# Optimization experiments

Hardware: AMD Instinct MI355X
Metric: run time of the kernel (lower is better)

The kernel has to match this reference:

```python
import jax, jax.numpy as jnp
import numpy as np

GAMMA = 1.0

def _rbf_mean(X, Y, gamma):
    x2 = jnp.sum(X * X, axis=1)  # [n]
    y2 = jnp.sum(Y * Y, axis=1)  # [m]
    d2 = x2[:, None] + y2[None, :] - 2.0 * (X @ Y.T)
    d2 = jnp.maximum(d2, 0.0)
    return jnp.mean(jnp.exp(-gamma * d2))

def setup_inputs() -> dict:
    key = jax.random.key(0)
    k1, k2 = jax.random.split(key)
    N = jax.random.normal(k1, (8192, 256), dtype=jnp.float32)
    R = jax.random.normal(k2, (8192, 256), dtype=jnp.float32)
    return {"N": N, "R": R}

def reference(N, R):
    xx = _rbf_mean(N, N, GAMMA)
    yy = _rbf_mean(R, R, GAMMA)
    xy = _rbf_mean(N, R, GAMMA)
    mmd = xx + yy - 2.0 * xy
    return jnp.sqrt(mmd)
```

## Files before the change

### kernel.cpp

```cpp
#include <hip/hip_runtime.h>
#include <math.h>

typedef float f32x4 __attribute__((ext_vector_type(4)));
typedef int   i32x4 __attribute__((ext_vector_type(4)));
typedef int   i32x8 __attribute__((ext_vector_type(8)));
typedef float f32x2 __attribute__((ext_vector_type(2)));

#define MTOT 16384
#define HALF 8192
#define KDIM 256
#define BM 256
#define NB (MTOT / BM)
#define NBLK (NB * (NB + 1) / 2)
#define NBLOCKS 256
#define TPX (NBLK / 8)

#define GLDS16(g, l) __builtin_amdgcn_global_load_lds(                      \
    (const __attribute__((address_space(1))) void*)(g),                     \
    (__attribute__((address_space(3))) void*)(l), 16, 0, 0)

#define BAR() do { asm volatile("" ::: "memory");                           \
  __builtin_amdgcn_s_barrier(); asm volatile("" ::: "memory"); } while (0)

__global__ __launch_bounds__(256) void convert_kernel(
    const float* __restrict__ Nmat, const float* __restrict__ Rmat,
    unsigned int* __restrict__ Z, float* __restrict__ x2,
    float* __restrict__ accum, unsigned int* __restrict__ counter) {
  if (blockIdx.x == 0 && threadIdx.x == 0) { *accum = 0.f; *counter = 0u; }
  const int lane = threadIdx.x & 63;
  const int wv = threadIdx.x >> 6;
  const int row = blockIdx.x * 4 + wv;
  const float* src = (row < HALF) ? (Nmat + (size_t)row * KDIM)
                                  : (Rmat + (size_t)(row - HALF) * KDIM);
  float4 v = *(const float4*)(src + lane * 4);
  int pk = __builtin_amdgcn_cvt_pk_fp8_f32(v.x, v.y, 0, false);
  pk = __builtin_amdgcn_cvt_pk_fp8_f32(v.z, v.w, pk, true);
  Z[(size_t)row * (KDIM / 4) + lane] = (unsigned int)pk;
  f32x2 d01 = __builtin_amdgcn_cvt_pk_f32_fp8(pk, false);
  f32x2 d23 = __builtin_amdgcn_cvt_pk_f32_fp8(pk, true);
  float sq = d01[0] * d01[0] + d01[1] * d01[1] + d23[0] * d23[0] + d23[1] * d23[1];
  #pragma unroll
  for (int off = 32; off; off >>= 1) sq += __shfl_down(sq, off);
  if (lane == 0) x2[row] = sq;
}

__device__ __forceinline__ void decode_tile(int t, int& bm, int& bn) {
  const int u = NBLK - 1 - t;
  int rr = (int)((sqrtf(8.0f * (float)u + 1.0f) - 1.0f) * 0.5f);
  while (rr * (rr + 1) / 2 > u) --rr;
  while ((rr + 1) * (rr + 2) / 2 <= u) ++rr;
  bm = NB - 1 - rr;
  bn = bm + (t - (bm * NB - bm * (bm - 1) / 2));
}

__global__ __launch_bounds__(512, 2) void mmd_gemm(
    const unsigned char* __restrict__ Z, const float* __restrict__ x2,
    float* __restrict__ accum, unsigned int* __restrict__ counter,
    float* __restrict__ out) {
  __shared__ unsigned char As[2 * 32768];
  __shared__ unsigned char Bs[2 * 32768];
  __shared__ float wsred[8];

  const int tid  = threadIdx.x;
  const int lane = tid & 63;
  const int wid  = tid >> 6;
  const int wm   = wid >> 2;
  const int wn   = wid & 3;

  const int lr = lane >> 3;
  const int ls = lane & 7;
  const int cofs = lr * KDIM + ((ls ^ lr) << 4);

  const int fr = lane & 15;
  const int fq = lane >> 4;
  const int key = fr & 7;
  const int slotL = ((2 * fq) ^ key) * 16;
  const int slotH = ((2 * fq + 1) ^ key) * 16;

  const int xcd = blockIdx.x & 7;
  const int lb  = blockIdx.x >> 3;
  const int niter = (lb < (TPX & 31)) ? (TPX / 32 + 1) : (TPX / 32);
  const int nslab = 2 * niter;

  f32x4 acc[8][4];

  auto STAGE = [&](int bmv, int bnv, int h, int buf) {
    const unsigned char* Ab = Z + (size_t)bmv * (BM * KDIM) + h * 128 + cofs;
    const unsigned char* Bb = Z + (size_t)bnv * (BM * KDIM) + h * 128 + cofs;
    unsigned char* Ad = As + buf * 32768;
    unsigned char* Bd = Bs + buf * 32768;
    #pragma unroll
    for (int tt = 0; tt < 4; ++tt) {
      int i = wid * 4 + tt;
      GLDS16(Ab + i * 2048, Ad + i * 1024);
      GLDS16(Bb + i * 2048, Bd + i * 1024);
    }
  };

  auto ACCINIT = [&](int bmv, int bnv) {
    float xch[4];
    #pragma unroll
    for (int tn = 0; tn < 4; ++tn)
      xch[tn] = -0.5f * x2[bnv * BM + wn * 64 + tn * 16 + fr];
    #pragma unroll
    for (int tm = 0; tm < 8; ++tm) {
      float4 xr = *(const float4*)(x2 + bmv * BM + wm * 128 + tm * 16 + fq * 4);
      #pragma unroll
      for (int tn = 0; tn < 4; ++tn) {
        acc[tm][tn][0] = -0.5f * xr.x + xch[tn];
        acc[tm][tn][1] = -0.5f * xr.y + xch[tn];
        acc[tm][tn][2] = -0.5f * xr.z + xch[tn];
        acc[tm][tn][3] = -0.5f * xr.w + xch[tn];
      }
    }
  };

  int cbm, cbn;
  decode_tile(xcd * TPX + lb, cbm, cbn);
  STAGE(cbm, cbn, 0, 0);
  STAGE(cbm, cbn, 1, 1);
  ACCINIT(cbm, cbn);
  int nbm = cbm, nbn = cbn;

  for (int j = 0; j < nslab; ++j) {
    const int bsel = j & 1;
    if (j + 1 < nslab) asm volatile("s_waitcnt vmcnt(8)" ::: "memory");
    else               asm volatile("s_waitcnt vmcnt(0)" ::: "memory");
    BAR();

    if (bsel == 0 && j > 0 && tid == 0) {
      float bs = 0.f;
      #pragma unroll
      for (int w = 0; w < 8; ++w) bs += wsred[w];
      atomicAdd(accum, bs);
    }

    {
      const unsigned char* A_s = As + bsel * 32768;
      const unsigned char* B_s = Bs + bsel * 32768;
      i32x8 bf[4];
      #pragma unroll
      for (int tn = 0; tn < 4; ++tn) {
        int row = wn * 64 + tn * 16 + fr;
        i32x4 lo = *(const i32x4*)(B_s + row * 128 + slotL);
        i32x4 hi = *(const i32x4*)(B_s + row * 128 + slotH);
        bf[tn] = __builtin_shufflevector(lo, hi, 0, 1, 2, 3, 4, 5, 6, 7);
      }
      #pragma unroll
      for (int tm = 0; tm < 8; ++tm) {
        int row = wm * 128 + tm * 16 + fr;
        i32x4 lo = *(const i32x4*)(A_s + row * 128 + slotL);
        i32x4 hi = *(const i32x4*)(A_s + row * 128 + slotH);
        i32x8 af = __builtin_shufflevector(lo, hi, 0, 1, 2, 3, 4, 5, 6, 7);
        #pragma unroll
        for (int tn = 0; tn < 4; ++tn)
          acc[tm][tn] = __builtin_amdgcn_mfma_scale_f32_16x16x128_f8f6f4(
              af, bf[tn], acc[tm][tn], 0, 0,
              0, 0x7F7F7F7F, 0, 0x7F7F7F7F);
      }
    }
    BAR();

    if (j + 2 < nslab) {
      if (bsel == 0) decode_tile(xcd * TPX + lb + 32 * ((j >> 1) + 1), nbm, nbn);
      STAGE(nbm, nbn, bsel , bsel);
    }

    if (bsel == 1) {
      float amax = -1e30f;
      #pragma unroll
      for (int tm = 0; tm < 8; ++tm)
        #pragma unroll
        for (int tn = 0; tn < 4; ++tn)
          #pragma unroll
          for (int v = 0; v < 4; ++v)
            amax = fmaxf(amax, acc[tm][tn][v]);

      float partial = 0.f;
      if (__any(amax > -40.f)) {
        #pragma unroll
        for (int tm = 0; tm < 8; ++tm)
          #pragma unroll
          for (int tn = 0; tn < 4; ++tn)
            #pragma unroll
            for (int v = 0; v < 4; ++v) {
              float a = fminf(acc[tm][tn][v], 0.f);
              partial += exp2f(a * 2.885390082f);
            }
      }
      #pragma unroll
      for (int off = 32; off; off >>= 1) partial += __shfl_down(partial, off);
      float wgt = ((cbm < NB / 2) == (cbn < NB / 2)) ? 1.f : -1.f;
      if (cbm != cbn) wgt *= 2.f;
      if (lane == 0) wsred[wid] = partial * wgt;
      asm volatile("s_waitcnt lgkmcnt(0)" ::: "memory");

      if (j + 2 < nslab) { ACCINIT(nbm, nbn); cbm = nbm; cbn = nbn; }
    }
  }

  BAR();
  if (tid == 0) {
    float bs = 0.f;
    #pragma unroll
    for (int w = 0; w < 8; ++w) bs += wsred[w];
    atomicAdd(accum, bs);
    __threadfence();
    unsigned int old = atomicAdd(counter, 1u);
    if (old == NBLOCKS - 1) {
      float tot = atomicAdd(accum, 0.f);
      float mmd = tot / ((float)HALF * (float)HALF);
      out[0] = sqrtf(fmaxf(mmd, 0.f));
    }
  }
}

extern "C" void kernel_launch(void* const* d_in, const int* in_sizes, int n_in,
                              void* d_out, int out_size, void* d_ws, size_t ws_size,
                              hipStream_t stream) {
  const float* Nmat = (const float*)d_in[0];
  const float* Rmat = (const float*)d_in[1];
  float* out = (float*)d_out;

  char* ws = (char*)d_ws;
  unsigned char* Z = (unsigned char*)ws;
  float* x2        = (float*)(ws + (size_t)MTOT * KDIM);
  float* accum     = (float*)(ws + (size_t)MTOT * KDIM + (size_t)MTOT * 4);
  unsigned int* counter = (unsigned int*)(ws + (size_t)MTOT * KDIM + (size_t)MTOT * 4 + 4);

  convert_kernel<<<MTOT / 4, 256, 0, stream>>>(Nmat, Rmat, (unsigned int*)Z, x2,
                                               accum, counter);
  mmd_gemm<<<NBLOCKS, 512, 0, stream>>>(Z, x2, accum, counter, out);
}
```

Baseline: 122.0 us.

## Stage row norms via async LDS loads and defer per-tile reductions

The -0.5 scaling of the squared norms moves into the convert kernel. The GEMM kernel now prefetches each tile's norms into double-buffered LDS with global_load_lds alongside the operand slabs, replacing direct global reads in the accumulator init. Per-tile wave shuffles, LDS writes and atomics are replaced by a per-thread running sum that is reduced once at the end. This removes global-latency stalls and per-tile reduction and sync overhead, but depends on hand-tuned vmcnt counts that must match the issued loads exactly.

Result: slower. 126.0 us (+3.3%).

```diff
diff --git a/kernel.cpp b/kernel.cpp
--- a/kernel.cpp
+++ b/kernel.cpp
@@ -41,7 +41,7 @@
   float sq = d01[0] * d01[0] + d01[1] * d01[1] + d23[0] * d23[0] + d23[1] * d23[1];
   #pragma unroll
   for (int off = 32; off; off >>= 1) sq += __shfl_down(sq, off);
-  if (lane == 0) x2[row] = sq;
+  if (lane == 0) x2[row] = -0.5f * sq;
 }
 
 __device__ __forceinline__ void decode_tile(int t, int& bm, int& bn) {
@@ -57,9 +57,10 @@
     const unsigned char* __restrict__ Z, const float* __restrict__ x2,
     float* __restrict__ accum, unsigned int* __restrict__ counter,
     float* __restrict__ out) {
-  __shared__ unsigned char As[2 * 32768];
-  __shared__ unsigned char Bs[2 * 32768];
-  __shared__ float wsred[8];
+  __shared__ __align__(16) unsigned char As[2 * 32768];
+  __shared__ __align__(16) unsigned char Bs[2 * 32768];
+  __shared__ __align__(16) float x2h[2][512];
+  __shared__ __align__(16) float wsred[8];
 
   const int tid  = threadIdx.x;
   const int lane = tid & 63;
@@ -83,6 +84,7 @@
   const int nslab = 2 * niter;
 
   f32x4 acc[8][4];
+  float running = 0.f;
 
   auto STAGE = [&](int bmv, int bnv, int h, int buf) {
     const unsigned char* Ab = Z + (size_t)bmv * (BM * KDIM) + h * 128 + cofs;
@@ -97,43 +99,46 @@
     }
   };
 
-  auto ACCINIT = [&](int bmv, int bnv) {
+  auto STAGEX2 = [&](int bmv, int bnv, int par) {
+    GLDS16((const unsigned char*)(x2 + bmv * BM) + lane * 16,
+           (unsigned char*)&x2h[par][0]);
+    GLDS16((const unsigned char*)(x2 + bnv * BM) + lane * 16,
+           (unsigned char*)&x2h[par][256]);
+  };
+
+  auto ACCINIT = [&](int par) {
     float xch[4];
     #pragma unroll
     for (int tn = 0; tn < 4; ++tn)
-      xch[tn] = -0.5f * x2[bnv * BM + wn * 64 + tn * 16 + fr];
+      xch[tn] = x2h[par][256 + wn * 64 + tn * 16 + fr];
     #pragma unroll
     for (int tm = 0; tm < 8; ++tm) {
-      float4 xr = *(const float4*)(x2 + bmv * BM + wm * 128 + tm * 16 + fq * 4);
-      #pragma unroll
-      for (int tn = 0; tn < 4; ++tn) {
-        acc[tm][tn][0] = -0.5f * xr.x + xch[tn];
-        acc[tm][tn][1] = -0.5f * xr.y + xch[tn];
-        acc[tm][tn][2] = -0.5f * xr.z + xch[tn];
-        acc[tm][tn][3] = -0.5f * xr.w + xch[tn];
-      }
+      f32x4 xr = *(const f32x4*)&x2h[par][wm * 128 + tm * 16 + fq * 4];
+      #pragma unroll
+      for (int tn = 0; tn < 4; ++tn)
+        #pragma unroll
+        for (int v = 0; v < 4; ++v)
+          acc[tm][tn][v] = xr[v] + xch[tn];
     }
   };
 
   int cbm, cbn;
   decode_tile(xcd * TPX + lb, cbm, cbn);
+  int nbm = cbm, nbn = cbn;
+  int cpar = 0;
+
+  STAGEX2(cbm, cbn, 0);
   STAGE(cbm, cbn, 0, 0);
   STAGE(cbm, cbn, 1, 1);
-  ACCINIT(cbm, cbn);
-  int nbm = cbm, nbn = cbn;
+  asm volatile("s_waitcnt vmcnt(16)" ::: "memory");
+  ACCINIT(0);
 
   for (int j = 0; j < nslab; ++j) {
     const int bsel = j & 1;
-    if (j + 1 < nslab) asm volatile("s_waitcnt vmcnt(8)" ::: "memory");
-    else               asm volatile("s_waitcnt vmcnt(0)" ::: "memory");
+    if (j + 1 >= nslab)      asm volatile("s_waitcnt vmcnt(0)" ::: "memory");
+    else if (bsel == 0)      asm volatile("s_waitcnt vmcnt(8)" ::: "memory");
+    else                     asm volatile("s_waitcnt vmcnt(10)" ::: "memory");
     BAR();
-
-    if (bsel == 0 && j > 0 && tid == 0) {
-      float bs = 0.f;
-      #pragma unroll
-      for (int w = 0; w < 8; ++w) bs += wsred[w];
-      atomicAdd(accum, bs);
-    }
 
     {
       const unsigned char* A_s = As + bsel * 32768;
@@ -162,8 +167,13 @@
     BAR();
 
     if (j + 2 < nslab) {
-      if (bsel == 0) decode_tile(xcd * TPX + lb + 32 * ((j >> 1) + 1), nbm, nbn);
-      STAGE(nbm, nbn, bsel , bsel);
+      if (bsel == 0) {
+        decode_tile(xcd * TPX + lb + 32 * ((j >> 1) + 1), nbm, nbn);
+        STAGEX2(nbm, nbn, cpar ^ 1);
+        STAGE(nbm, nbn, 0, 0);
+      } else {
+        STAGE(nbm, nbn, 1, 1);
+      }
     }
 
     if (bsel == 1) {
@@ -171,10 +181,10 @@
       #pragma unroll
       for (int tm = 0; tm < 8; ++tm)
         #pragma unroll
-        for (int tn = 0; tn < 4; ++tn)
-          #pragma unroll
-          for (int v = 0; v < 4; ++v)
-            amax = fmaxf(amax, acc[tm][tn][v]);
+        for (int tn = 0; tn < 4; ++tn) {
+          float m1 = fmaxf(fmaxf(acc[tm][tn][0], acc[tm][tn][1]), acc[tm][tn][2]);
+          amax = fmaxf(fmaxf(amax, m1), acc[tm][tn][3]);
+        }
 
       float partial = 0.f;
       if (__any(amax > -40.f)) {
@@ -188,18 +198,23 @@
               partial += exp2f(a * 2.885390082f);
             }
       }
-      #pragma unroll
-      for (int off = 32; off; off >>= 1) partial += __shfl_down(partial, off);
       float wgt = ((cbm < NB / 2) == (cbn < NB / 2)) ? 1.f : -1.f;
       if (cbm != cbn) wgt *= 2.f;
-      if (lane == 0) wsred[wid] = partial * wgt;
-      asm volatile("s_waitcnt lgkmcnt(0)" ::: "memory");
-
-      if (j + 2 < nslab) { ACCINIT(nbm, nbn); cbm = nbm; cbn = nbn; }
+      running += partial * wgt;
+
+      if (j + 2 < nslab) {
+        asm volatile("s_waitcnt vmcnt(16)" ::: "memory");
+        cpar ^= 1;
+        ACCINIT(cpar);
+        cbm = nbm; cbn = nbn;
+      }
     }
   }
 
-  BAR();
+  #pragma unroll
+  for (int off = 32; off; off >>= 1) running += __shfl_down(running, off);
+  if (lane == 0) wsred[wid] = running;
+  __syncthreads();
   if (tid == 0) {
     float bs = 0.f;
     #pragma unroll
```
